# Kernel optimization log

Hardware: AMD Instinct MI355X
Metric: run time of the kernel (lower is better)

The kernel has to match this reference:

```python
import jax, jax.numpy as jnp
import numpy as np

EPS = 1e-5
CLUSTER_COUNT = 64
B, N, DV, DA = 128, 300, 1024, 128


def setup_inputs() -> dict:
    key = jax.random.key(0)
    k1, k2 = jax.random.split(key)
    video = jax.random.normal(k1, (B, N, DV), dtype=jnp.float32)
    audio = jax.random.normal(k2, (B, N, DA), dtype=jnp.float32)
    return {"video": video, "audio": audio}


def _select_indices(x_norm):
    """Greedy farthest-point (min |cosine|) selection for one batch. x_norm: [N, D]."""
    # indices starts as [0]; first appended index comes from sims of row 0
    best = jnp.abs(x_norm @ x_norm[0])          # [N]
    last = jnp.argmin(best)

    def step(carry, _):
        best, last = carry
        sims = jnp.abs(x_norm @ x_norm[last])   # [N]
        best = jnp.maximum(best, sims)
        new_last = jnp.argmin(best)
        return (best, new_last), new_last

    (_, _), rest = jax.lax.scan(step, (best, last), None, length=CLUSTER_COUNT - 2)
    idx = jnp.concatenate([jnp.array([0], dtype=last.dtype),
                           last[None], rest])  # [CLUSTER_COUNT]
    return jnp.sort(idx)


def reference(video, audio):
    # video: [B, N, DV], audio: [B, N, DA]
    norm = jnp.linalg.norm(video, axis=2) + EPS          # [B, N]
    video_normalized = video / norm[:, :, None]
    idx = jax.vmap(_select_indices)(video_normalized)     # [B, K], sorted
    v_sel = jnp.take_along_axis(video, idx[:, :, None], axis=1)  # [B, K, DV]
    a_sel = jnp.take_along_axis(audio, idx[:, :, None], axis=1)  # [B, K, DA]
    return v_sel, a_sel
```

## Files before the change

kernel.cpp:

```cpp
#include <hip/hip_runtime.h>
#include <math.h>


constexpr int BB = 128, NN = 300, DV = 1024, DA = 128, KK = 64;
constexpr int TRI = NN * (NN + 1) / 2;
constexpr int KC = 32;
constexpr int NCH = DV / KC;
constexpr int LDH = 36;

constexpr int GS = 304;
constexpr int GBATCH = NN * GS;
constexpr size_t SQ_NEED = (size_t)BB * GBATCH * 4;

constexpr int NT2 = 6;
__device__ __constant__ int t2_ib[NT2] = {0,0,0,1,1,2};
__device__ __constant__ int t2_jb[NT2] = {0,1,2,1,2,2};

constexpr int NTILES = 15;
constexpr int TB = 64;
__device__ __constant__ int c_ib[NTILES] = {0,0,0,0,0, 1,1,1,1, 2,2,2, 3,3, 4};
__device__ __constant__ int c_jb[NTILES] = {0,1,2,3,4, 1,2,3,4, 2,3,4, 3,4, 4};

typedef _Float16 f16x8 __attribute__((ext_vector_type(8)));
typedef float    f32x4 __attribute__((ext_vector_type(4)));

union H4 { _Float16 h[4]; uint2 u; };
union F8 { uint2 u2[2]; f16x8 v; };

__device__ __forceinline__ int tri_base(int i) { return i * NN - (i * (i - 1)) / 2; }

__global__ __launch_bounds__(512, 4) void kgram3(const float* __restrict__ video,
                                                 float* __restrict__ G) {
    const int bid  = blockIdx.x;
    const int swz  = (bid & 7) * 96 + (bid >> 3);
    const int batch = swz / NT2;
    const int tile  = swz - batch * NT2;
    const int i0 = t2_ib[tile] * 128, j0 = t2_jb[tile] * 128;
    const bool diag = (i0 == j0);
    const int tid = threadIdx.x;

    __shared__ _Float16 sH[2][4][128][LDH];
    __shared__ float    s_part[512];
    __shared__ double   s_inv[2][128];

    const float* vb = video + (size_t)batch * NN * DV;

    const int slab  = tid >> 8;
    const int st    = tid & 255;
    const int lrow  = st >> 1;
    const int khalf = st & 1;
    const int grow  = (slab ? j0 : i0) + lrow;
    const bool rok  = grow < NN;
    const bool stage_on = !(diag && slab == 1);
    const float4* srcb4 = (const float4*)(vb + (size_t)(rok ? grow : 0) * DV);
    const int qbase = khalf * 4;

    const int lane = tid & 63, w = tid >> 6;
    const int wr2 = w >> 2, wc2 = w & 3;
    const int g = lane >> 4, c16 = lane & 15;
    const int bplane = diag ? 0 : 2;

    f32x4 acc[4][2];
    #pragma unroll
    for (int fr = 0; fr < 4; ++fr)
        #pragma unroll
        for (int fc = 0; fc < 2; ++fc) acc[fr][fc] = (f32x4){0.f, 0.f, 0.f, 0.f};

    float ps = 0.f;
    float4 ld[4];
    const float4 z4 = make_float4(0.f, 0.f, 0.f, 0.f);

    auto stage_write = [&](int bf) {
        #pragma unroll
        for (int q = 0; q < 4; ++q) {
            float4 v = ld[q];
            ps = fmaf(v.x, v.x, fmaf(v.y, v.y, fmaf(v.z, v.z, fmaf(v.w, v.w, ps))));
            H4 hi, lo;
            _Float16 h0 = (_Float16)v.x, h1 = (_Float16)v.y,
                     h2 = (_Float16)v.z, h3 = (_Float16)v.w;
            hi.h[0] = h0; hi.h[1] = h1; hi.h[2] = h2; hi.h[3] = h3;
            lo.h[0] = (_Float16)(v.x - (float)h0);
            lo.h[1] = (_Float16)(v.y - (float)h1);
            lo.h[2] = (_Float16)(v.z - (float)h2);
            lo.h[3] = (_Float16)(v.w - (float)h3);
            const int p = khalf * 16 + 4 * q;
            *(uint2*)&sH[bf][slab * 2 + 0][lrow][p] = hi.u;
            *(uint2*)&sH[bf][slab * 2 + 1][lrow][p] = lo.u;
        }
    };

    if (stage_on) {
        #pragma unroll
        for (int q = 0; q < 4; ++q) ld[q] = rok ? srcb4[qbase + q] : z4;
        stage_write(0);
        #pragma unroll
        for (int q = 0; q < 4; ++q) ld[q] = rok ? srcb4[8 + qbase + q] : z4;
    }
    __syncthreads();

    for (int kc = 0; kc < NCH; ++kc) {
        const int cur = kc & 1, nxt = cur ^ 1;
        if (stage_on && kc < NCH - 1) stage_write(nxt);
        if (stage_on && kc < NCH - 2) {
            #pragma unroll
            for (int q = 0; q < 4; ++q)
                ld[q] = rok ? srcb4[(kc + 2) * 8 + qbase + q] : z4;
        }

        f16x8 Ah[4], Al[4], Bh[2], Bl[2];
        #pragma unroll
        for (int fr = 0; fr < 4; ++fr) {
            const int row = 64 * wr2 + 16 * fr + c16;
            F8 t;
            t.u2[0] = *(const uint2*)&sH[cur][0][row][4 * g];
            t.u2[1] = *(const uint2*)&sH[cur][0][row][16 + 4 * g];
            Ah[fr] = t.v;
            t.u2[0] = *(const uint2*)&sH[cur][1][row][4 * g];
            t.u2[1] = *(const uint2*)&sH[cur][1][row][16 + 4 * g];
            Al[fr] = t.v;
        }
        #pragma unroll
        for (int fc = 0; fc < 2; ++fc) {
            const int row = 32 * wc2 + 16 * fc + c16;
            F8 t;
            t.u2[0] = *(const uint2*)&sH[cur][bplane + 0][row][4 * g];
            t.u2[1] = *(const uint2*)&sH[cur][bplane + 0][row][16 + 4 * g];
            Bh[fc] = t.v;
            t.u2[0] = *(const uint2*)&sH[cur][bplane + 1][row][4 * g];
            t.u2[1] = *(const uint2*)&sH[cur][bplane + 1][row][16 + 4 * g];
            Bl[fc] = t.v;
        }
        #pragma unroll
        for (int fr = 0; fr < 4; ++fr)
            #pragma unroll
            for (int fc = 0; fc < 2; ++fc) {
                acc[fr][fc] = __builtin_amdgcn_mfma_f32_16x16x32_f16(Ah[fr], Bh[fc], acc[fr][fc], 0, 0, 0);
                acc[fr][fc] = __builtin_amdgcn_mfma_f32_16x16x32_f16(Ah[fr], Bl[fc], acc[fr][fc], 0, 0, 0);
                acc[fr][fc] = __builtin_amdgcn_mfma_f32_16x16x32_f16(Al[fr], Bh[fc], acc[fr][fc], 0, 0, 0);
            }
        __syncthreads();
    }

    s_part[tid] = ps;
    __syncthreads();
    if (tid < 256) {
        const int sl = tid >> 7, r = tid & 127;
        const int src = (sl && !diag) ? 256 + 2 * r : 2 * r;
        float ssum = s_part[src] + s_part[src + 1];
        s_inv[sl][r] = 1.0 / (sqrt((double)ssum) + 1e-5);
    }
    __syncthreads();

    float* Gb = G + (size_t)batch * GBATCH;
    #pragma unroll
    for (int fr = 0; fr < 4; ++fr)
        #pragma unroll
        for (int fc = 0; fc < 2; ++fc)
            #pragma unroll
            for (int reg = 0; reg < 4; ++reg) {
                const int il = 64 * wr2 + 16 * fr + 4 * g + reg;
                const int jl = 32 * wc2 + 16 * fc + c16;
                const int i = i0 + il, j = j0 + jl;
                if (i <= j && j < NN) {
                    float val = (float)(fabs((double)acc[fr][fc][reg]) *
                                        s_inv[0][il] * s_inv[1][jl]);
                    Gb[i * GS + j] = val;
                    Gb[j * GS + i] = val;
                }
            }
}

__global__ __launch_bounds__(256) void kgram_lds(const float* __restrict__ video,
                                                 float* __restrict__ G) {
    const int bid  = blockIdx.x;
    const int swz  = (bid & 7) * 240 + (bid >> 3);
    const int batch = swz / 15;
    const int tile  = swz - batch * 15;
    const int i0 = c_ib[tile] * TB, j0 = c_jb[tile] * TB;
    const bool diag = (i0 == j0);
    const int tid = threadIdx.x;

    __shared__ _Float16 sH[2][4][TB][LDH];
    __shared__ float    s_part[256];
    __shared__ double   s_inv[2][TB];

    const float* vb = video + (size_t)batch * NN * DV;

    const int slab  = tid >> 7;
    const int lrow  = (tid >> 1) & 63;
    const int khalf = tid & 1;
    const int grow  = (slab ? j0 : i0) + lrow;
    const bool rok  = grow < NN;
    const bool stage_on = !(diag && slab == 1);
    const float4* srcb4 = (const float4*)(vb + (size_t)(rok ? grow : 0) * DV);
    const int qbase = khalf * 4;

    const int lane = tid & 63, w = tid >> 6;
    const int wr = w >> 1, wc = w & 1;
    const int g = lane >> 4, c16 = lane & 15;
    const int bplane = diag ? 0 : 2;

    f32x4 acc[2][2];
    #pragma unroll
    for (int fr = 0; fr < 2; ++fr)
        #pragma unroll
        for (int fc = 0; fc < 2; ++fc) acc[fr][fc] = (f32x4){0.f, 0.f, 0.f, 0.f};

    float ps = 0.f;
    float4 ld[4];
    const float4 z4 = make_float4(0.f, 0.f, 0.f, 0.f);

    auto stage_write = [&](int bf) {
        #pragma unroll
        for (int q = 0; q < 4; ++q) {
            float4 v = ld[q];
            ps = fmaf(v.x, v.x, fmaf(v.y, v.y, fmaf(v.z, v.z, fmaf(v.w, v.w, ps))));
            H4 hi, lo;
            _Float16 h0 = (_Float16)v.x, h1 = (_Float16)v.y,
                     h2 = (_Float16)v.z, h3 = (_Float16)v.w;
            hi.h[0] = h0; hi.h[1] = h1; hi.h[2] = h2; hi.h[3] = h3;
            lo.h[0] = (_Float16)(v.x - (float)h0);
            lo.h[1] = (_Float16)(v.y - (float)h1);
            lo.h[2] = (_Float16)(v.z - (float)h2);
            lo.h[3] = (_Float16)(v.w - (float)h3);
            const int p = khalf * 16 + 4 * q;
            *(uint2*)&sH[bf][slab * 2 + 0][lrow][p] = hi.u;
            *(uint2*)&sH[bf][slab * 2 + 1][lrow][p] = lo.u;
        }
    };

    if (stage_on) {
        #pragma unroll
        for (int q = 0; q < 4; ++q) ld[q] = rok ? srcb4[qbase + q] : z4;
        stage_write(0);
        #pragma unroll
        for (int q = 0; q < 4; ++q) ld[q] = rok ? srcb4[8 + qbase + q] : z4;
    }
    __syncthreads();

    for (int kc = 0; kc < NCH; ++kc) {
        const int cur = kc & 1, nxt = cur ^ 1;
        if (stage_on && kc < NCH - 1) stage_write(nxt);
        if (stage_on && kc < NCH - 2) {
            #pragma unroll
            for (int q = 0; q < 4; ++q)
                ld[q] = rok ? srcb4[(kc + 2) * 8 + qbase + q] : z4;
        }

        f16x8 Ah[2], Al[2], Bh[2], Bl[2];
        #pragma unroll
        for (int fr = 0; fr < 2; ++fr) {
            const int row = 32 * wr + 16 * fr + c16;
            F8 t;
            t.u2[0] = *(const uint2*)&sH[cur][0][row][4 * g];
            t.u2[1] = *(const uint2*)&sH[cur][0][row][16 + 4 * g];
            Ah[fr] = t.v;
            t.u2[0] = *(const uint2*)&sH[cur][1][row][4 * g];
            t.u2[1] = *(const uint2*)&sH[cur][1][row][16 + 4 * g];
            Al[fr] = t.v;
        }
        #pragma unroll
        for (int fc = 0; fc < 2; ++fc) {
            const int row = 32 * wc + 16 * fc + c16;
            F8 t;
            t.u2[0] = *(const uint2*)&sH[cur][bplane + 0][row][4 * g];
            t.u2[1] = *(const uint2*)&sH[cur][bplane + 0][row][16 + 4 * g];
            Bh[fc] = t.v;
            t.u2[0] = *(const uint2*)&sH[cur][bplane + 1][row][4 * g];
            t.u2[1] = *(const uint2*)&sH[cur][bplane + 1][row][16 + 4 * g];
            Bl[fc] = t.v;
        }
        #pragma unroll
        for (int fr = 0; fr < 2; ++fr)
            #pragma unroll
            for (int fc = 0; fc < 2; ++fc) {
                acc[fr][fc] = __builtin_amdgcn_mfma_f32_16x16x32_f16(Ah[fr], Bh[fc], acc[fr][fc], 0, 0, 0);
                acc[fr][fc] = __builtin_amdgcn_mfma_f32_16x16x32_f16(Ah[fr], Bl[fc], acc[fr][fc], 0, 0, 0);
                acc[fr][fc] = __builtin_amdgcn_mfma_f32_16x16x32_f16(Al[fr], Bh[fc], acc[fr][fc], 0, 0, 0);
            }
        __syncthreads();
    }

    s_part[tid] = ps;
    __syncthreads();
    if (tid < 128) {
        const int sl = tid >> 6, r = tid & 63;
        const int src = (sl && !diag) ? 128 + 2 * r : 2 * r;
        float ssum = s_part[src] + s_part[src + 1];
        s_inv[sl][r] = 1.0 / (sqrt((double)ssum) + 1e-5);
    }
    __syncthreads();

    float* Gb = G + (size_t)batch * TRI;
    #pragma unroll
    for (int fr = 0; fr < 2; ++fr)
        #pragma unroll
        for (int fc = 0; fc < 2; ++fc)
            #pragma unroll
            for (int reg = 0; reg < 4; ++reg) {
                const int il = 32 * wr + 16 * fr + 4 * g + reg;
                const int jl = 32 * wc + 16 * fc + c16;
                const int i = i0 + il, j = j0 + jl;
                if (i <= j && j < NN)
                    Gb[tri_base(i) + (j - i)] =
                        (float)(fabs((double)acc[fr][fc][reg]) * s_inv[0][il] * s_inv[1][jl]);
            }
}

__device__ __forceinline__ void select_wave_sq(const float* __restrict__ Gb,
                                               int lane, int* s_sorted) {
    float best[5];
    int myidx = 0;

    #pragma unroll
    for (int q = 0; q < 5; ++q) {
        int r = lane + 64 * q;
        best[q] = (r < NN) ? Gb[r] : 3.4e38f;
    }

    int last;
    {
        float v = INFINITY; int ri = 1 << 30;
        #pragma unroll
        for (int q = 0; q < 5; ++q)
            if (best[q] < v) { v = best[q]; ri = lane + 64 * q; }
        #pragma unroll
        for (int off = 32; off >= 1; off >>= 1) {
            float ov = __shfl_xor(v, off, 64); int oi = __shfl_xor(ri, off, 64);
            if (ov < v || (ov == v && oi < ri)) { v = ov; ri = oi; }
        }
        last = ri;
    }
    if (lane == 1) myidx = last;

    for (int t = 2; t < KK; ++t) {
        const float* row = Gb + last * GS;
        #pragma unroll
        for (int q = 0; q < 5; ++q) {
            int r = lane + 64 * q;
            if (r < NN) best[q] = fmaxf(best[q], row[r]);
        }
        float v = INFINITY; int ri = 1 << 30;
        #pragma unroll
        for (int q = 0; q < 5; ++q)
            if (best[q] < v) { v = best[q]; ri = lane + 64 * q; }
        #pragma unroll
        for (int off = 32; off >= 1; off >>= 1) {
            float ov = __shfl_xor(v, off, 64); int oi = __shfl_xor(ri, off, 64);
            if (ov < v || (ov == v && oi < ri)) { v = ov; ri = oi; }
        }
        last = ri;
        if (lane == t) myidx = last;
    }

    int rank = 0;
    for (int j = 0; j < KK; ++j) {
        int oj = __shfl(myidx, j, 64);
        rank += (oj < myidx) || (oj == myidx && j < lane);
    }
    s_sorted[rank] = myidx;
}

__device__ __forceinline__ void select_wave_tri(const float* __restrict__ Gb,
                                                int lane, int* s_sorted) {
    float best[5];
    int myidx = 0;

    #pragma unroll
    for (int q = 0; q < 5; ++q) {
        int r = lane + 64 * q;
        best[q] = (r < NN) ? Gb[r] : 3.4e38f;
    }

    int last;
    {
        float v = INFINITY; int ri = 1 << 30;
        #pragma unroll
        for (int q = 0; q < 5; ++q)
            if (best[q] < v) { v = best[q]; ri = lane + 64 * q; }
        #pragma unroll
        for (int off = 32; off >= 1; off >>= 1) {
            float ov = __shfl_xor(v, off, 64); int oi = __shfl_xor(ri, off, 64);
            if (ov < v || (ov == v && oi < ri)) { v = ov; ri = oi; }
        }
        last = ri;
    }
    if (lane == 1) myidx = last;

    for (int t = 2; t < KK; ++t) {
        #pragma unroll
        for (int q = 0; q < 5; ++q) {
            int r = lane + 64 * q;
            if (r < NN) {
                int i = min(last, r), j = max(last, r);
                best[q] = fmaxf(best[q], Gb[tri_base(i) + (j - i)]);
            }
        }
        float v = INFINITY; int ri = 1 << 30;
        #pragma unroll
        for (int q = 0; q < 5; ++q)
            if (best[q] < v) { v = best[q]; ri = lane + 64 * q; }
        #pragma unroll
        for (int off = 32; off >= 1; off >>= 1) {
            float ov = __shfl_xor(v, off, 64); int oi = __shfl_xor(ri, off, 64);
            if (ov < v || (ov == v && oi < ri)) { v = ov; ri = oi; }
        }
        last = ri;
        if (lane == t) myidx = last;
    }

    int rank = 0;
    for (int j = 0; j < KK; ++j) {
        int oj = __shfl(myidx, j, 64);
        rank += (oj < myidx) || (oj == myidx && j < lane);
    }
    s_sorted[rank] = myidx;
}

__global__ __launch_bounds__(256) void kfused_sq(const float* __restrict__ G,
                                                 const float* __restrict__ video,
                                                 const float* __restrict__ audio,
                                                 float* __restrict__ out_v,
                                                 float* __restrict__ out_a) {
    const int b = blockIdx.x, tid = threadIdx.x;
    __shared__ int s_sorted[KK];

    if (tid < 64)
        select_wave_sq(G + (size_t)b * GBATCH, tid, s_sorted);
    __syncthreads();

    const float4* vb4 = (const float4*)(video + (size_t)b * NN * DV);
    float4* ov4 = (float4*)(out_v + (size_t)b * KK * DV);
    #pragma unroll 4
    for (int t = tid; t < KK * DV / 4; t += 256) {
        int k = t >> 8, c = t & 255;
        ov4[t] = vb4[s_sorted[k] * (DV / 4) + c];
    }
    const float4* ab4 = (const float4*)(audio + (size_t)b * NN * DA);
    float4* oa4 = (float4*)(out_a + (size_t)b * KK * DA);
    for (int t = tid; t < KK * DA / 4; t += 256) {
        int k = t >> 5, c = t & 31;
        oa4[t] = ab4[s_sorted[k] * (DA / 4) + c];
    }
}

__global__ __launch_bounds__(256) void kfused_tri(const float* __restrict__ G,
                                                  const float* __restrict__ video,
                                                  const float* __restrict__ audio,
                                                  float* __restrict__ out_v,
                                                  float* __restrict__ out_a) {
    const int b = blockIdx.x, tid = threadIdx.x;
    __shared__ int s_sorted[KK];

    if (tid < 64)
        select_wave_tri(G + (size_t)b * TRI, tid, s_sorted);
    __syncthreads();

    const float4* vb4 = (const float4*)(video + (size_t)b * NN * DV);
    float4* ov4 = (float4*)(out_v + (size_t)b * KK * DV);
    #pragma unroll 4
    for (int t = tid; t < KK * DV / 4; t += 256) {
        int k = t >> 8, c = t & 255;
        ov4[t] = vb4[s_sorted[k] * (DV / 4) + c];
    }
    const float4* ab4 = (const float4*)(audio + (size_t)b * NN * DA);
    float4* oa4 = (float4*)(out_a + (size_t)b * KK * DA);
    for (int t = tid; t < KK * DA / 4; t += 256) {
        int k = t >> 5, c = t & 31;
        oa4[t] = ab4[s_sorted[k] * (DA / 4) + c];
    }
}

__global__ __launch_bounds__(64) void kselect(const float* __restrict__ G,
                                              float* __restrict__ out_a) {
    __shared__ int s_sorted[KK];
    select_wave_tri(G + (size_t)blockIdx.x * TRI, threadIdx.x, s_sorted);
    __syncthreads();
    ((int*)(out_a + (size_t)blockIdx.x * KK * DA))[threadIdx.x] = s_sorted[threadIdx.x];
}

__global__ __launch_bounds__(256) void kgather(const float* __restrict__ video,
                                               const float* __restrict__ audio,
                                               float* __restrict__ out_v,
                                               float* __restrict__ out_a) {
    int b = blockIdx.x, tid = threadIdx.x;
    __shared__ int s_idx[KK];
    const int* idxp = (const int*)(out_a + (size_t)b * KK * DA);
    if (tid < KK) s_idx[tid] = idxp[tid];
    __syncthreads();

    const float4* vb4 = (const float4*)(video + (size_t)b * NN * DV);
    float4* ov4 = (float4*)(out_v + (size_t)b * KK * DV);
    #pragma unroll 4
    for (int t = tid; t < KK * DV / 4; t += 256) {
        int k = t >> 8, c = t & 255;
        ov4[t] = vb4[s_idx[k] * (DV / 4) + c];
    }
    const float4* ab4 = (const float4*)(audio + (size_t)b * NN * DA);
    float4* oa4 = (float4*)(out_a + (size_t)b * KK * DA);
    for (int t = tid; t < KK * DA / 4; t += 256) {
        int k = t >> 5, c = t & 31;
        oa4[t] = ab4[s_idx[k] * (DA / 4) + c];
    }
}

extern "C" void kernel_launch(void* const* d_in, const int* in_sizes, int n_in,
                              void* d_out, int out_size, void* d_ws, size_t ws_size,
                              hipStream_t stream) {
    const float* video = (const float*)d_in[0];
    const float* audio = (const float*)d_in[1];
    float* out   = (float*)d_out;
    float* out_v = out;
    float* out_a = out + (size_t)BB * KK * DV;

    const size_t tri_bytes = (size_t)BB * TRI * sizeof(float);

    if (ws_size >= SQ_NEED) {
        float* G = (float*)d_ws;
        kgram3   <<<NT2 * BB, 512, 0, stream>>>(video, G);
        kfused_sq<<<BB, 256, 0, stream>>>(G, video, audio, out_v, out_a);
    } else if (ws_size >= tri_bytes) {
        float* G = (float*)d_ws;
        kgram_lds <<<NTILES * BB, 256, 0, stream>>>(video, G);
        kfused_tri<<<BB, 256, 0, stream>>>(G, video, audio, out_v, out_a);
    } else {
        float* G = out;
        kgram_lds<<<NTILES * BB, 256, 0, stream>>>(video, G);
        kselect  <<<BB, 64, 0, stream>>>(G, out_a);
        kgather  <<<BB, 256, 0, stream>>>(video, audio, out_v, out_a);
    }
}
```

Before: 214.6 us.

## Single-buffer gram LDS staging and split select from gather kernels

The 128x128 gram kernel moves from a double-buffered LDS staging scheme to a single buffer with a register prefetch of one chunk and an extra barrier per k-step. The intent is to halve LDS use so more blocks fit per CU. The fused select+gather kernel is split in two. A 64-thread select kernel writes the indices to workspace, and a gather kernel runs on 2x as many blocks to spread the copy across more CUs instead of idling 192 threads during selection. This adds a launch, a round trip through workspace for the indices, and a larger workspace requirement that could make the fast path fall back.

After: 263.7 us. 22.9% more time.

```diff
diff --git a/kernel.cpp b/kernel.cpp
--- a/kernel.cpp
+++ b/kernel.cpp
@@ -10,7 +10,9 @@
 
 constexpr int GS = 304;
 constexpr int GBATCH = NN * GS;
-constexpr size_t SQ_NEED = (size_t)BB * GBATCH * 4;
+constexpr size_t SQ_BYTES = (size_t)BB * GBATCH * 4;
+constexpr size_t IDX_OFF  = SQ_BYTES;
+constexpr size_t SQ_NEED  = SQ_BYTES + (size_t)BB * KK * 4;
 
 constexpr int NT2 = 6;
 __device__ __constant__ int t2_ib[NT2] = {0,0,0,1,1,2};
@@ -29,8 +31,8 @@
 
 __device__ __forceinline__ int tri_base(int i) { return i * NN - (i * (i - 1)) / 2; }
 
-__global__ __launch_bounds__(512, 4) void kgram3(const float* __restrict__ video,
-                                                 float* __restrict__ G) {
+__global__ __launch_bounds__(512, 4) void kgram3s(const float* __restrict__ video,
+                                                  float* __restrict__ G) {
     const int bid  = blockIdx.x;
     const int swz  = (bid & 7) * 96 + (bid >> 3);
     const int batch = swz / NT2;
@@ -39,7 +41,7 @@
     const bool diag = (i0 == j0);
     const int tid = threadIdx.x;
 
-    __shared__ _Float16 sH[2][4][128][LDH];
+    __shared__ _Float16 sH[4][128][LDH];
     __shared__ float    s_part[512];
     __shared__ double   s_inv[2][128];
 
@@ -63,6 +65,144 @@
     f32x4 acc[4][2];
     #pragma unroll
     for (int fr = 0; fr < 4; ++fr)
+        #pragma unroll
+        for (int fc = 0; fc < 2; ++fc) acc[fr][fc] = (f32x4){0.f, 0.f, 0.f, 0.f};
+
+    float ps = 0.f;
+    float4 ld[4];
+    const float4 z4 = make_float4(0.f, 0.f, 0.f, 0.f);
+
+    auto stage_write = [&]() {
+        #pragma unroll
+        for (int q = 0; q < 4; ++q) {
+            float4 v = ld[q];
+            ps = fmaf(v.x, v.x, fmaf(v.y, v.y, fmaf(v.z, v.z, fmaf(v.w, v.w, ps))));
+            H4 hi, lo;
+            _Float16 h0 = (_Float16)v.x, h1 = (_Float16)v.y,
+                     h2 = (_Float16)v.z, h3 = (_Float16)v.w;
+            hi.h[0] = h0; hi.h[1] = h1; hi.h[2] = h2; hi.h[3] = h3;
+            lo.h[0] = (_Float16)(v.x - (float)h0);
+            lo.h[1] = (_Float16)(v.y - (float)h1);
+            lo.h[2] = (_Float16)(v.z - (float)h2);
+            lo.h[3] = (_Float16)(v.w - (float)h3);
+            const int p = khalf * 16 + 4 * q;
+            *(uint2*)&sH[slab * 2 + 0][lrow][p] = hi.u;
+            *(uint2*)&sH[slab * 2 + 1][lrow][p] = lo.u;
+        }
+    };
+
+    if (stage_on) {
+        #pragma unroll
+        for (int q = 0; q < 4; ++q) ld[q] = rok ? srcb4[qbase + q] : z4;
+    }
+
+    for (int kc = 0; kc < NCH; ++kc) {
+        if (stage_on) {
+            stage_write();
+            if (kc < NCH - 1) {
+                #pragma unroll
+                for (int q = 0; q < 4; ++q)
+                    ld[q] = rok ? srcb4[(kc + 1) * 8 + qbase + q] : z4;
+            }
+        }
+        __syncthreads();
+
+        f16x8 Ah[4], Al[4], Bh[2], Bl[2];
+        #pragma unroll
+        for (int fr = 0; fr < 4; ++fr) {
+            const int row = 64 * wr2 + 16 * fr + c16;
+            F8 t;
+            t.u2[0] = *(const uint2*)&sH[0][row][4 * g];
+            t.u2[1] = *(const uint2*)&sH[0][row][16 + 4 * g];
+            Ah[fr] = t.v;
+            t.u2[0] = *(const uint2*)&sH[1][row][4 * g];
+            t.u2[1] = *(const uint2*)&sH[1][row][16 + 4 * g];
+            Al[fr] = t.v;
+        }
+        #pragma unroll
+        for (int fc = 0; fc < 2; ++fc) {
+            const int row = 32 * wc2 + 16 * fc + c16;
+            F8 t;
+            t.u2[0] = *(const uint2*)&sH[bplane + 0][row][4 * g];
+            t.u2[1] = *(const uint2*)&sH[bplane + 0][row][16 + 4 * g];
+            Bh[fc] = t.v;
+            t.u2[0] = *(const uint2*)&sH[bplane + 1][row][4 * g];
+            t.u2[1] = *(const uint2*)&sH[bplane + 1][row][16 + 4 * g];
+            Bl[fc] = t.v;
+        }
+        #pragma unroll
+        for (int fr = 0; fr < 4; ++fr)
+            #pragma unroll
+            for (int fc = 0; fc < 2; ++fc) {
+                acc[fr][fc] = __builtin_amdgcn_mfma_f32_16x16x32_f16(Ah[fr], Bh[fc], acc[fr][fc], 0, 0, 0);
+                acc[fr][fc] = __builtin_amdgcn_mfma_f32_16x16x32_f16(Ah[fr], Bl[fc], acc[fr][fc], 0, 0, 0);
+                acc[fr][fc] = __builtin_amdgcn_mfma_f32_16x16x32_f16(Al[fr], Bh[fc], acc[fr][fc], 0, 0, 0);
+            }
+        __syncthreads();
+    }
+
+    s_part[tid] = ps;
+    __syncthreads();
+    if (tid < 256) {
+        const int sl = tid >> 7, r = tid & 127;
+        const int src = (sl && !diag) ? 256 + 2 * r : 2 * r;
+        float ssum = s_part[src] + s_part[src + 1];
+        s_inv[sl][r] = 1.0 / (sqrt((double)ssum) + 1e-5);
+    }
+    __syncthreads();
+
+    float* Gb = G + (size_t)batch * GBATCH;
+    #pragma unroll
+    for (int fr = 0; fr < 4; ++fr)
+        #pragma unroll
+        for (int fc = 0; fc < 2; ++fc)
+            #pragma unroll
+            for (int reg = 0; reg < 4; ++reg) {
+                const int il = 64 * wr2 + 16 * fr + 4 * g + reg;
+                const int jl = 32 * wc2 + 16 * fc + c16;
+                const int i = i0 + il, j = j0 + jl;
+                if (i <= j && j < NN) {
+                    float val = (float)(fabs((double)acc[fr][fc][reg]) *
+                                        s_inv[0][il] * s_inv[1][jl]);
+                    Gb[i * GS + j] = val;
+                    Gb[j * GS + i] = val;
+                }
+            }
+}
+
+__global__ __launch_bounds__(256) void kgram_lds(const float* __restrict__ video,
+                                                 float* __restrict__ G) {
+    const int bid  = blockIdx.x;
+    const int swz  = (bid & 7) * 240 + (bid >> 3);
+    const int batch = swz / 15;
+    const int tile  = swz - batch * 15;
+    const int i0 = c_ib[tile] * TB, j0 = c_jb[tile] * TB;
+    const bool diag = (i0 == j0);
+    const int tid = threadIdx.x;
+
+    __shared__ _Float16 sH[2][4][TB][LDH];
+    __shared__ float    s_part[256];
+    __shared__ double   s_inv[2][TB];
+
+    const float* vb = video + (size_t)batch * NN * DV;
+
+    const int slab  = tid >> 7;
+    const int lrow  = (tid >> 1) & 63;
+    const int khalf = tid & 1;
+    const int grow  = (slab ? j0 : i0) + lrow;
+    const bool rok  = grow < NN;
+    const bool stage_on = !(diag && slab == 1);
+    const float4* srcb4 = (const float4*)(vb + (size_t)(rok ? grow : 0) * DV);
+    const int qbase = khalf * 4;
+
+    const int lane = tid & 63, w = tid >> 6;
+    const int wr = w >> 1, wc = w & 1;
+    const int g = lane >> 4, c16 = lane & 15;
+    const int bplane = diag ? 0 : 2;
+
+    f32x4 acc[2][2];
+    #pragma unroll
+    for (int fr = 0; fr < 2; ++fr)
         #pragma unroll
         for (int fc = 0; fc < 2; ++fc) acc[fr][fc] = (f32x4){0.f, 0.f, 0.f, 0.f};
 
@@ -107,146 +247,6 @@
                 ld[q] = rok ? srcb4[(kc + 2) * 8 + qbase + q] : z4;
         }
 
-        f16x8 Ah[4], Al[4], Bh[2], Bl[2];
-        #pragma unroll
-        for (int fr = 0; fr < 4; ++fr) {
-            const int row = 64 * wr2 + 16 * fr + c16;
-            F8 t;
-            t.u2[0] = *(const uint2*)&sH[cur][0][row][4 * g];
-            t.u2[1] = *(const uint2*)&sH[cur][0][row][16 + 4 * g];
-            Ah[fr] = t.v;
-            t.u2[0] = *(const uint2*)&sH[cur][1][row][4 * g];
-            t.u2[1] = *(const uint2*)&sH[cur][1][row][16 + 4 * g];
-            Al[fr] = t.v;
-        }
-        #pragma unroll
-        for (int fc = 0; fc < 2; ++fc) {
-            const int row = 32 * wc2 + 16 * fc + c16;
-            F8 t;
-            t.u2[0] = *(const uint2*)&sH[cur][bplane + 0][row][4 * g];
-            t.u2[1] = *(const uint2*)&sH[cur][bplane + 0][row][16 + 4 * g];
-            Bh[fc] = t.v;
-            t.u2[0] = *(const uint2*)&sH[cur][bplane + 1][row][4 * g];
-            t.u2[1] = *(const uint2*)&sH[cur][bplane + 1][row][16 + 4 * g];
-            Bl[fc] = t.v;
-        }
-        #pragma unroll
-        for (int fr = 0; fr < 4; ++fr)
-            #pragma unroll
-            for (int fc = 0; fc < 2; ++fc) {
-                acc[fr][fc] = __builtin_amdgcn_mfma_f32_16x16x32_f16(Ah[fr], Bh[fc], acc[fr][fc], 0, 0, 0);
-                acc[fr][fc] = __builtin_amdgcn_mfma_f32_16x16x32_f16(Ah[fr], Bl[fc], acc[fr][fc], 0, 0, 0);
-                acc[fr][fc] = __builtin_amdgcn_mfma_f32_16x16x32_f16(Al[fr], Bh[fc], acc[fr][fc], 0, 0, 0);
-            }
-        __syncthreads();
-    }
-
-    s_part[tid] = ps;
-    __syncthreads();
-    if (tid < 256) {
-        const int sl = tid >> 7, r = tid & 127;
-        const int src = (sl && !diag) ? 256 + 2 * r : 2 * r;
-        float ssum = s_part[src] + s_part[src + 1];
-        s_inv[sl][r] = 1.0 / (sqrt((double)ssum) + 1e-5);
-    }
-    __syncthreads();
-
-    float* Gb = G + (size_t)batch * GBATCH;
-    #pragma unroll
-    for (int fr = 0; fr < 4; ++fr)
-        #pragma unroll
-        for (int fc = 0; fc < 2; ++fc)
-            #pragma unroll
-            for (int reg = 0; reg < 4; ++reg) {
-                const int il = 64 * wr2 + 16 * fr + 4 * g + reg;
-                const int jl = 32 * wc2 + 16 * fc + c16;
-                const int i = i0 + il, j = j0 + jl;
-                if (i <= j && j < NN) {
-                    float val = (float)(fabs((double)acc[fr][fc][reg]) *
-                                        s_inv[0][il] * s_inv[1][jl]);
-                    Gb[i * GS + j] = val;
-                    Gb[j * GS + i] = val;
-                }
-            }
-}
-
-__global__ __launch_bounds__(256) void kgram_lds(const float* __restrict__ video,
-                                                 float* __restrict__ G) {
-    const int bid  = blockIdx.x;
-    const int swz  = (bid & 7) * 240 + (bid >> 3);
-    const int batch = swz / 15;
-    const int tile  = swz - batch * 15;
-    const int i0 = c_ib[tile] * TB, j0 = c_jb[tile] * TB;
-    const bool diag = (i0 == j0);
-    const int tid = threadIdx.x;
-
-    __shared__ _Float16 sH[2][4][TB][LDH];
-    __shared__ float    s_part[256];
-    __shared__ double   s_inv[2][TB];
-
-    const float* vb = video + (size_t)batch * NN * DV;
-
-    const int slab  = tid >> 7;
-    const int lrow  = (tid >> 1) & 63;
-    const int khalf = tid & 1;
-    const int grow  = (slab ? j0 : i0) + lrow;
-    const bool rok  = grow < NN;
-    const bool stage_on = !(diag && slab == 1);
-    const float4* srcb4 = (const float4*)(vb + (size_t)(rok ? grow : 0) * DV);
-    const int qbase = khalf * 4;
-
-    const int lane = tid & 63, w = tid >> 6;
-    const int wr = w >> 1, wc = w & 1;
-    const int g = lane >> 4, c16 = lane & 15;
-    const int bplane = diag ? 0 : 2;
-
-    f32x4 acc[2][2];
-    #pragma unroll
-    for (int fr = 0; fr < 2; ++fr)
-        #pragma unroll
-        for (int fc = 0; fc < 2; ++fc) acc[fr][fc] = (f32x4){0.f, 0.f, 0.f, 0.f};
-
-    float ps = 0.f;
-    float4 ld[4];
-    const float4 z4 = make_float4(0.f, 0.f, 0.f, 0.f);
-
-    auto stage_write = [&](int bf) {
-        #pragma unroll
-        for (int q = 0; q < 4; ++q) {
-            float4 v = ld[q];
-            ps = fmaf(v.x, v.x, fmaf(v.y, v.y, fmaf(v.z, v.z, fmaf(v.w, v.w, ps))));
-            H4 hi, lo;
-            _Float16 h0 = (_Float16)v.x, h1 = (_Float16)v.y,
-                     h2 = (_Float16)v.z, h3 = (_Float16)v.w;
-            hi.h[0] = h0; hi.h[1] = h1; hi.h[2] = h2; hi.h[3] = h3;
-            lo.h[0] = (_Float16)(v.x - (float)h0);
-            lo.h[1] = (_Float16)(v.y - (float)h1);
-            lo.h[2] = (_Float16)(v.z - (float)h2);
-            lo.h[3] = (_Float16)(v.w - (float)h3);
-            const int p = khalf * 16 + 4 * q;
-            *(uint2*)&sH[bf][slab * 2 + 0][lrow][p] = hi.u;
-            *(uint2*)&sH[bf][slab * 2 + 1][lrow][p] = lo.u;
-        }
-    };
-
-    if (stage_on) {
-        #pragma unroll
-        for (int q = 0; q < 4; ++q) ld[q] = rok ? srcb4[qbase + q] : z4;
-        stage_write(0);
-        #pragma unroll
-        for (int q = 0; q < 4; ++q) ld[q] = rok ? srcb4[8 + qbase + q] : z4;
-    }
-    __syncthreads();
-
-    for (int kc = 0; kc < NCH; ++kc) {
-        const int cur = kc & 1, nxt = cur ^ 1;
-        if (stage_on && kc < NCH - 1) stage_write(nxt);
-        if (stage_on && kc < NCH - 2) {
-            #pragma unroll
-            for (int q = 0; q < 4; ++q)
-                ld[q] = rok ? srcb4[(kc + 2) * 8 + qbase + q] : z4;
-        }
-
         f16x8 Ah[2], Al[2], Bh[2], Bl[2];
         #pragma unroll
         for (int fr = 0; fr < 2; ++fr) {
@@ -417,30 +417,38 @@
     s_sorted[rank] = myidx;
 }
 
-__global__ __launch_bounds__(256) void kfused_sq(const float* __restrict__ G,
-                                                 const float* __restrict__ video,
-                                                 const float* __restrict__ audio,
-                                                 float* __restrict__ out_v,
-                                                 float* __restrict__ out_a) {
-    const int b = blockIdx.x, tid = threadIdx.x;
+__global__ __launch_bounds__(64) void ksel_sq(const float* __restrict__ G,
+                                              int* __restrict__ idx) {
     __shared__ int s_sorted[KK];
-
-    if (tid < 64)
-        select_wave_sq(G + (size_t)b * GBATCH, tid, s_sorted);
+    select_wave_sq(G + (size_t)blockIdx.x * GBATCH, threadIdx.x, s_sorted);
+    __syncthreads();
+    idx[blockIdx.x * KK + threadIdx.x] = s_sorted[threadIdx.x];
+}
+
+__global__ __launch_bounds__(256) void kgath(const int* __restrict__ idx,
+                                             const float* __restrict__ video,
+                                             const float* __restrict__ audio,
+                                             float* __restrict__ out_v,
+                                             float* __restrict__ out_a) {
+    const int b = blockIdx.x >> 1, half = blockIdx.x & 1, tid = threadIdx.x;
+    __shared__ int s_idx[KK];
+    if (tid < KK) s_idx[tid] = idx[b * KK + tid];
     __syncthreads();
 
     const float4* vb4 = (const float4*)(video + (size_t)b * NN * DV);
     float4* ov4 = (float4*)(out_v + (size_t)b * KK * DV);
+    const int vbeg = half * 8192, vend = vbeg + 8192;
     #pragma unroll 4
-    for (int t = tid; t < KK * DV / 4; t += 256) {
+    for (int t = vbeg + tid; t < vend; t += 256) {
         int k = t >> 8, c = t & 255;
-        ov4[t] = vb4[s_sorted[k] * (DV / 4) + c];
+        ov4[t] = vb4[s_idx[k] * (DV / 4) + c];
     }
     const float4* ab4 = (const float4*)(audio + (size_t)b * NN * DA);
     float4* oa4 = (float4*)(out_a + (size_t)b * KK * DA);
-    for (int t = tid; t < KK * DA / 4; t += 256) {
+    const int abeg = half * 1024, aend = abeg + 1024;
+    for (int t = abeg + tid; t < aend; t += 256) {
         int k = t >> 5, c = t & 31;
-        oa4[t] = ab4[s_sorted[k] * (DA / 4) + c];
+        oa4[t] = ab4[s_idx[k] * (DA / 4) + c];
     }
 }
 
@@ -517,8 +525,10 @@
 
     if (ws_size >= SQ_NEED) {
         float* G = (float*)d_ws;
-        kgram3   <<<NT2 * BB, 512, 0, stream>>>(video, G);
-        kfused_sq<<<BB, 256, 0, stream>>>(G, video, audio, out_v, out_a);
+        int* idx = (int*)((char*)d_ws + IDX_OFF);
+        kgram3s<<<NT2 * BB, 512, 0, stream>>>(video, G);
+        ksel_sq<<<BB, 64, 0, stream>>>(G, idx);
+        kgath  <<<2 * BB, 256, 0, stream>>>(idx, video, audio, out_v, out_a);
     } else if (ws_size >= tri_bytes) {
         float* G = (float*)d_ws;
         kgram_lds <<<NTILES * BB, 256, 0, stream>>>(video, G);
```
